# Kernel optimization log

Hardware: AMD Instinct MI355X
Metric: run time of the kernel (lower is better)

## Reference

```python
import jax, jax.numpy as jnp
import numpy as np

LD, LU, N, D_IN, D_OUT, K = 16384, 65536, 8, 256, 128, 3


def setup_inputs() -> dict:
    key = jax.random.key(0)
    ks = jax.random.split(key, 7)
    down_features = jax.random.normal(ks[0], (LD, N, D_IN), dtype=jnp.float32)
    up_features = jax.random.normal(ks[1], (LU, N, D_OUT), dtype=jnp.float32)
    idx = jax.random.randint(ks[2], (LU, N, K), 0, LD, dtype=jnp.int32)
    W1 = jax.random.normal(ks[3], (D_IN, D_OUT), dtype=jnp.float32) / np.sqrt(D_IN)
    b1 = jnp.zeros((D_OUT,), dtype=jnp.float32)
    W2 = jax.random.normal(ks[4], (D_OUT, D_OUT), dtype=jnp.float32) / np.sqrt(D_OUT)
    b2 = jnp.zeros((D_OUT,), dtype=jnp.float32)
    return {"down_features": down_features, "up_features": up_features, "idx": idx,
            "W1": W1, "b1": b1, "W2": W2, "b2": b2}


def reference(down_features, up_features, idx, W1, b1, W2, b2):
    # MLP: Linear(d, d_out) -> ReLU -> Linear(d_out, d_out), applied per point
    h = jax.nn.relu(jnp.einsum("lnd,de->lne", down_features, W1) + b1)
    h = jnp.einsum("lnd,de->lne", h, W2) + b2            # (Ld, N, Du)
    # KNN upsample: gather K neighbors per upsampled point, average, residual add
    n = jnp.arange(h.shape[1])[None, :, None]            # (1, N, 1) batch index
    gathered = h[idx, n, :]                              # (Lu, N, K, Du)
    up = up_features + gathered.mean(axis=2)             # (Lu, N, Du)
    return up
```

## Files before the change

kernel.cpp:

```cpp
#include <hip/hip_runtime.h>

#define LD_   16384
#define LU_   65536
#define N_    8
#define DIN   256
#define DOUT  128
#define K_    3
#define M_    (LD_ * N_)

typedef short bf16x8 __attribute__((ext_vector_type(8)));
typedef float f32x4  __attribute__((ext_vector_type(4)));
typedef unsigned int u32x2 __attribute__((ext_vector_type(2)));

__device__ __forceinline__ unsigned short f2bf(float f) {
    unsigned int x = __float_as_uint(f);
    x += 0x7fffu + ((x >> 16) & 1u);
    return (unsigned short)(x >> 16);
}

__device__ __forceinline__ bf16x8 ld_bf16x8(const unsigned short* p) {
    const short4 lo = *(const short4*)p;
    const short4 hi = *(const short4*)(p + 4);
    bf16x8 r = {lo.x, lo.y, lo.z, lo.w, hi.x, hi.y, hi.z, hi.w};
    return r;
}

#define W1_STRIDE 264
#define W2_STRIDE 132
#define H1_STRIDE 132

__global__ __launch_bounds__(512, 2) void knn_mlp_mfma(
    const float* __restrict__ down, const float* __restrict__ W1,
    const float* __restrict__ b1,   const float* __restrict__ W2,
    const float* __restrict__ b2,   unsigned short* __restrict__ h)
{
    __shared__ unsigned short sW1t[DOUT * W1_STRIDE];
    __shared__ unsigned short sW2t[DOUT * W2_STRIDE];
    __shared__ unsigned short sH[8][16 * H1_STRIDE];

    const int tid = threadIdx.x;

    #pragma unroll
    for (int it = 0; it < 16; ++it) {
        const int fid = it * 512 + tid;
        const int k = fid >> 5, n4 = (fid & 31) * 4;
        const float4 w = ((const float4*)W1)[fid];
        sW1t[(n4 + 0) * W1_STRIDE + k] = f2bf(w.x);
        sW1t[(n4 + 1) * W1_STRIDE + k] = f2bf(w.y);
        sW1t[(n4 + 2) * W1_STRIDE + k] = f2bf(w.z);
        sW1t[(n4 + 3) * W1_STRIDE + k] = f2bf(w.w);
    }
    #pragma unroll
    for (int it = 0; it < 8; ++it) {
        const int fid = it * 512 + tid;
        const int k = fid >> 5, n4 = (fid & 31) * 4;
        const float4 w = ((const float4*)W2)[fid];
        sW2t[(n4 + 0) * W2_STRIDE + k] = f2bf(w.x);
        sW2t[(n4 + 1) * W2_STRIDE + k] = f2bf(w.y);
        sW2t[(n4 + 2) * W2_STRIDE + k] = f2bf(w.z);
        sW2t[(n4 + 3) * W2_STRIDE + k] = f2bf(w.w);
    }
    __syncthreads();

    const int wave = tid >> 6, lane = tid & 63;
    const int lm = lane & 15, lg = lane >> 4;
    unsigned short* hw = sH[wave];

    float b1r[8], b2r[8];
    #pragma unroll
    for (int nt = 0; nt < 8; ++nt) {
        b1r[nt] = b1[nt * 16 + lm];
        b2r[nt] = b2[nt * 16 + lm];
    }

    const int row0 = blockIdx.x * 512 + wave * 16;
    const float* dbase = down + (size_t)(row0 + lm) * DIN + lg * 8;

    float4 raw[2][16];

    #pragma unroll
    for (int k = 0; k < 8; ++k) {
        raw[0][2 * k]     = *(const float4*)(dbase + k * 32);
        raw[0][2 * k + 1] = *(const float4*)(dbase + k * 32 + 4);
    }

    #pragma unroll
    for (int pass = 0; pass < 4; ++pass) {
        const int cur = pass & 1;
        const int chunk = row0 + pass * 128;

        if (pass < 3) {
            const float* dp = dbase + (size_t)(pass + 1) * 128 * DIN;
            #pragma unroll
            for (int k = 0; k < 8; ++k) {
                raw[cur ^ 1][2 * k]     = *(const float4*)(dp + k * 32);
                raw[cur ^ 1][2 * k + 1] = *(const float4*)(dp + k * 32 + 4);
            }
        }

        f32x4 acc[8];
        #pragma unroll
        for (int nt = 0; nt < 8; ++nt) acc[nt] = (f32x4){0.f, 0.f, 0.f, 0.f};
        #pragma unroll
        for (int k = 0; k < 8; ++k) {
            const float4 r0 = raw[cur][2 * k], r1 = raw[cur][2 * k + 1];
            const bf16x8 a = {(short)f2bf(r0.x), (short)f2bf(r0.y), (short)f2bf(r0.z), (short)f2bf(r0.w),
                              (short)f2bf(r1.x), (short)f2bf(r1.y), (short)f2bf(r1.z), (short)f2bf(r1.w)};
            const int koff = k * 32 + lg * 8;
            #pragma unroll
            for (int nt = 0; nt < 8; ++nt) {
                const bf16x8 B = ld_bf16x8(&sW1t[(nt * 16 + lm) * W1_STRIDE + koff]);
                acc[nt] = __builtin_amdgcn_mfma_f32_16x16x32_bf16(a, B, acc[nt], 0, 0, 0);
            }
        }

        #pragma unroll
        for (int nt = 0; nt < 8; ++nt) {
            #pragma unroll
            for (int i = 0; i < 4; ++i) {
                float v = acc[nt][i] + b1r[nt];
                v = fmaxf(v, 0.0f);
                hw[(lg * 4 + i) * H1_STRIDE + nt * 16 + lm] = f2bf(v);
            }
        }
        asm volatile("s_waitcnt lgkmcnt(0)" ::: "memory");

        f32x4 acc2[8];
        #pragma unroll
        for (int nt = 0; nt < 8; ++nt) acc2[nt] = (f32x4){0.f, 0.f, 0.f, 0.f};
        #pragma unroll
        for (int k = 0; k < 4; ++k) {
            const int koff = k * 32 + lg * 8;
            const bf16x8 A2 = ld_bf16x8(&hw[lm * H1_STRIDE + koff]);
            #pragma unroll
            for (int nt = 0; nt < 8; ++nt) {
                const bf16x8 B = ld_bf16x8(&sW2t[(nt * 16 + lm) * W2_STRIDE + koff]);
                acc2[nt] = __builtin_amdgcn_mfma_f32_16x16x32_bf16(A2, B, acc2[nt], 0, 0, 0);
            }
        }

        #pragma unroll
        for (int nt = 0; nt < 8; ++nt) {
            #pragma unroll
            for (int i = 0; i < 4; ++i) {
                const float v = acc2[nt][i] + b2r[nt];
                h[(size_t)(chunk + lg * 4 + i) * DOUT + nt * 16 + lm] = f2bf(v);
            }
        }
    }
}

__global__ __launch_bounds__(256) void knn_gather(
    const float* __restrict__ up, const int* __restrict__ idx,
    const unsigned int* __restrict__ h32, float* __restrict__ out)
{
    const int wave = threadIdx.x >> 6, lane = threadIdx.x & 63;
    const int half = lane >> 5, lih = lane & 31;
    const long long wid  = (long long)blockIdx.x * 4 + wave;
    const long long base = wid * 64;

    const int* ip = idx + (base + lane) * 3;
    const int mi0 = ip[0], mi1 = ip[1], mi2 = ip[2];

    const u32x2* hg   = (const u32x2*)h32;
    const f32x4* upv  = (const f32x4*)up;
    f32x4*       outv = (f32x4*)out;

    #pragma unroll
    for (int gb = 0; gb < 8; ++gb) {
        u32x2 ga[4][3];
        f32x4 uu[4];
        int   pp[4];
        #pragma unroll
        for (int u = 0; u < 4; ++u) {
            const int p = (gb * 4 + u) * 2 + half;
            pp[u] = p;
            const int i0 = __shfl(mi0, p);
            const int i1 = __shfl(mi1, p);
            const int i2 = __shfl(mi2, p);
            const int n  = p & 7;
            ga[u][0] = hg[(unsigned)(i0 * 8 + n) * 32u + lih];
            ga[u][1] = hg[(unsigned)(i1 * 8 + n) * 32u + lih];
            ga[u][2] = hg[(unsigned)(i2 * 8 + n) * 32u + lih];
            uu[u] = __builtin_nontemporal_load(&upv[(base + p) * 32 + lih]);
        }
        #pragma unroll
        for (int u = 0; u < 4; ++u) {
            float s0 = 0.f, s1 = 0.f, s2 = 0.f, s3 = 0.f;
            #pragma unroll
            for (int j = 0; j < 3; ++j) {
                const u32x2 v = ga[u][j];
                s0 += __uint_as_float(v.x << 16);
                s1 += __uint_as_float(v.x & 0xffff0000u);
                s2 += __uint_as_float(v.y << 16);
                s3 += __uint_as_float(v.y & 0xffff0000u);
            }
            f32x4 o;
            o.x = uu[u].x + s0 * (1.0f / 3.0f);
            o.y = uu[u].y + s1 * (1.0f / 3.0f);
            o.z = uu[u].z + s2 * (1.0f / 3.0f);
            o.w = uu[u].w + s3 * (1.0f / 3.0f);
            __builtin_nontemporal_store(o, &outv[(base + pp[u]) * 32 + lih]);
        }
    }
}

extern "C" void kernel_launch(void* const* d_in, const int* in_sizes, int n_in,
                              void* d_out, int out_size, void* d_ws, size_t ws_size,
                              hipStream_t stream)
{
    const float* down = (const float*)d_in[0];
    const float* up   = (const float*)d_in[1];
    const int*   idx  = (const int*)d_in[2];
    const float* W1   = (const float*)d_in[3];
    const float* b1   = (const float*)d_in[4];
    const float* W2   = (const float*)d_in[5];
    const float* b2   = (const float*)d_in[6];
    float* out = (float*)d_out;
    unsigned short* h = (unsigned short*)d_ws;

    knn_mlp_mfma<<<256, 512, 0, stream>>>(down, W1, b1, W2, b2, h);
    knn_gather<<<2048, 256, 0, stream>>>(up, idx, (const unsigned int*)h, out);
}
```

Before: 563.0 us.

## Transpose MFMA operands so outputs store as packed bf16x4 vectors

Swaps the A/B operands of the MFMA so each lane's accumulator holds four consecutive output columns of one row. This lets the hidden-layer write to LDS and the final h write to global memory use 8-byte vector stores instead of scattered 2-byte stores. Biases move to LDS and are read as float4. The raw input register double buffer becomes one buffer, with conversion to bf16 done before the next prefetch, which cuts register pressure but may shorten load latency hiding.

```diff
diff --git a/kernel.cpp b/kernel.cpp
--- a/kernel.cpp
+++ b/kernel.cpp
@@ -37,8 +37,21 @@
     __shared__ unsigned short sW1t[DOUT * W1_STRIDE];
     __shared__ unsigned short sW2t[DOUT * W2_STRIDE];
     __shared__ unsigned short sH[8][16 * H1_STRIDE];
-
-    const int tid = threadIdx.x;
+    __shared__ float sB1[DOUT], sB2[DOUT];
+
+    const int tid  = threadIdx.x;
+    const int wave = tid >> 6, lane = tid & 63;
+    const int lm = lane & 15, lg = lane >> 4;
+
+    const int row0 = blockIdx.x * 512 + wave * 16;
+    const float* dbase = down + (size_t)(row0 + lm) * DIN + lg * 8;
+
+    float4 raw[16];
+    #pragma unroll
+    for (int k = 0; k < 8; ++k) {
+        raw[2 * k]     = *(const float4*)(dbase + k * 32);
+        raw[2 * k + 1] = *(const float4*)(dbase + k * 32 + 4);
+    }
 
     #pragma unroll
     for (int it = 0; it < 16; ++it) {
@@ -60,41 +73,31 @@
         sW2t[(n4 + 2) * W2_STRIDE + k] = f2bf(w.z);
         sW2t[(n4 + 3) * W2_STRIDE + k] = f2bf(w.w);
     }
+    if (tid < 32)                 ((float4*)sB1)[tid]      = ((const float4*)b1)[tid];
+    else if (tid < 64)            ((float4*)sB2)[tid - 32] = ((const float4*)b2)[tid - 32];
     __syncthreads();
 
-    const int wave = tid >> 6, lane = tid & 63;
-    const int lm = lane & 15, lg = lane >> 4;
     unsigned short* hw = sH[wave];
 
-    float b1r[8], b2r[8];
-    #pragma unroll
-    for (int nt = 0; nt < 8; ++nt) {
-        b1r[nt] = b1[nt * 16 + lm];
-        b2r[nt] = b2[nt * 16 + lm];
-    }
-
-    const int row0 = blockIdx.x * 512 + wave * 16;
-    const float* dbase = down + (size_t)(row0 + lm) * DIN + lg * 8;
-
-    float4 raw[2][16];
-
-    #pragma unroll
-    for (int k = 0; k < 8; ++k) {
-        raw[0][2 * k]     = *(const float4*)(dbase + k * 32);
-        raw[0][2 * k + 1] = *(const float4*)(dbase + k * 32 + 4);
-    }
-
     #pragma unroll
     for (int pass = 0; pass < 4; ++pass) {
-        const int cur = pass & 1;
         const int chunk = row0 + pass * 128;
+
+        bf16x8 A[8];
+        #pragma unroll
+        for (int k = 0; k < 8; ++k) {
+            const float4 r0 = raw[2 * k], r1 = raw[2 * k + 1];
+            const bf16x8 a = {(short)f2bf(r0.x), (short)f2bf(r0.y), (short)f2bf(r0.z), (short)f2bf(r0.w),
+                              (short)f2bf(r1.x), (short)f2bf(r1.y), (short)f2bf(r1.z), (short)f2bf(r1.w)};
+            A[k] = a;
+        }
 
         if (pass < 3) {
             const float* dp = dbase + (size_t)(pass + 1) * 128 * DIN;
             #pragma unroll
             for (int k = 0; k < 8; ++k) {
-                raw[cur ^ 1][2 * k]     = *(const float4*)(dp + k * 32);
-                raw[cur ^ 1][2 * k + 1] = *(const float4*)(dp + k * 32 + 4);
+                raw[2 * k]     = *(const float4*)(dp + k * 32);
+                raw[2 * k + 1] = *(const float4*)(dp + k * 32 + 4);
             }
         }
 
@@ -103,25 +106,23 @@
         for (int nt = 0; nt < 8; ++nt) acc[nt] = (f32x4){0.f, 0.f, 0.f, 0.f};
         #pragma unroll
         for (int k = 0; k < 8; ++k) {
-            const float4 r0 = raw[cur][2 * k], r1 = raw[cur][2 * k + 1];
-            const bf16x8 a = {(short)f2bf(r0.x), (short)f2bf(r0.y), (short)f2bf(r0.z), (short)f2bf(r0.w),
-                              (short)f2bf(r1.x), (short)f2bf(r1.y), (short)f2bf(r1.z), (short)f2bf(r1.w)};
             const int koff = k * 32 + lg * 8;
             #pragma unroll
             for (int nt = 0; nt < 8; ++nt) {
-                const bf16x8 B = ld_bf16x8(&sW1t[(nt * 16 + lm) * W1_STRIDE + koff]);
-                acc[nt] = __builtin_amdgcn_mfma_f32_16x16x32_bf16(a, B, acc[nt], 0, 0, 0);
+                const bf16x8 Wf = ld_bf16x8(&sW1t[(nt * 16 + lm) * W1_STRIDE + koff]);
+                acc[nt] = __builtin_amdgcn_mfma_f32_16x16x32_bf16(Wf, A[k], acc[nt], 0, 0, 0);
             }
         }
 
         #pragma unroll
         for (int nt = 0; nt < 8; ++nt) {
-            #pragma unroll
-            for (int i = 0; i < 4; ++i) {
-                float v = acc[nt][i] + b1r[nt];
-                v = fmaxf(v, 0.0f);
-                hw[(lg * 4 + i) * H1_STRIDE + nt * 16 + lm] = f2bf(v);
-            }
+            const float4 bq = *(const float4*)&sB1[nt * 16 + lg * 4];
+            ushort4 st;
+            st.x = f2bf(fmaxf(acc[nt][0] + bq.x, 0.0f));
+            st.y = f2bf(fmaxf(acc[nt][1] + bq.y, 0.0f));
+            st.z = f2bf(fmaxf(acc[nt][2] + bq.z, 0.0f));
+            st.w = f2bf(fmaxf(acc[nt][3] + bq.w, 0.0f));
+            *(ushort4*)&hw[lm * H1_STRIDE + nt * 16 + lg * 4] = st;
         }
         asm volatile("s_waitcnt lgkmcnt(0)" ::: "memory");
 
@@ -129,23 +130,25 @@
         #pragma unroll
         for (int nt = 0; nt < 8; ++nt) acc2[nt] = (f32x4){0.f, 0.f, 0.f, 0.f};
         #pragma unroll
-        for (int k = 0; k < 4; ++k) {
-            const int koff = k * 32 + lg * 8;
-            const bf16x8 A2 = ld_bf16x8(&hw[lm * H1_STRIDE + koff]);
+        for (int ks = 0; ks < 4; ++ks) {
+            const int koff = ks * 32 + lg * 8;
+            const bf16x8 Bh = ld_bf16x8(&hw[lm * H1_STRIDE + koff]);
             #pragma unroll
             for (int nt = 0; nt < 8; ++nt) {
-                const bf16x8 B = ld_bf16x8(&sW2t[(nt * 16 + lm) * W2_STRIDE + koff]);
-                acc2[nt] = __builtin_amdgcn_mfma_f32_16x16x32_bf16(A2, B, acc2[nt], 0, 0, 0);
+                const bf16x8 Wf = ld_bf16x8(&sW2t[(nt * 16 + lm) * W2_STRIDE + koff]);
+                acc2[nt] = __builtin_amdgcn_mfma_f32_16x16x32_bf16(Wf, Bh, acc2[nt], 0, 0, 0);
             }
         }
 
         #pragma unroll
         for (int nt = 0; nt < 8; ++nt) {
-            #pragma unroll
-            for (int i = 0; i < 4; ++i) {
-                const float v = acc2[nt][i] + b2r[nt];
-                h[(size_t)(chunk + lg * 4 + i) * DOUT + nt * 16 + lm] = f2bf(v);
-            }
+            const float4 bq = *(const float4*)&sB2[nt * 16 + lg * 4];
+            ushort4 st;
+            st.x = f2bf(acc2[nt][0] + bq.x);
+            st.y = f2bf(acc2[nt][1] + bq.y);
+            st.z = f2bf(acc2[nt][2] + bq.z);
+            st.w = f2bf(acc2[nt][3] + bq.w);
+            *(ushort4*)&h[(size_t)(chunk + lm) * DOUT + nt * 16 + lg * 4] = st;
         }
     }
 }
```

Measured after the change: 554.7 us. About the same (-1.5%).
